# Kernel optimization log

Measured on AMD Instinct MI355X. Metric: run time of the kernel, lower is better.

Reference implementation:

```python
import jax, jax.numpy as jnp
import numpy as np

B, S = 2, 2048
H = 16
NOPE, ROPE, VD = 128, 64, 128
Q_RANK, KV_RANK = 1536, 512
SCALE = 1.0 / np.sqrt(NOPE + ROPE)  # 1/sqrt(192)
NEG_INF = -10000.0


def _make_rope(n_pos, dim):
    # matches gen_rope: theta over even indices, angles repeated twice (rotate-half layout)
    theta = 1.0 / (10000.0 ** (np.arange(0, dim, 2, dtype=np.float32) / dim))
    pos = np.arange(n_pos, dtype=np.float32)
    ang = np.outer(pos, theta)                      # [N, dim/2]
    ang = np.concatenate([ang, ang], axis=-1)       # [N, dim]
    return jnp.asarray(np.cos(ang)), jnp.asarray(np.sin(ang))


def _rope(x, cos, sin):
    # rotate-half RoPE; cos/sin broadcast over head dim if present
    d = x.shape[-1]
    x1, x2 = x[..., : d // 2], x[..., d // 2 :]
    rot = jnp.concatenate([-x2, x1], axis=-1)
    return x * cos + rot * sin


def setup_inputs() -> dict:
    key = jax.random.key(0)
    ks = jax.random.split(key, 5)
    Q = jax.random.normal(ks[0], (B, S, Q_RANK), dtype=jnp.float32)
    KV = jax.random.normal(ks[1], (B, S, KV_RANK), dtype=jnp.float32)
    PE = jax.random.normal(ks[2], (B, S, ROPE), dtype=jnp.float32)
    WUQ = jax.random.normal(ks[3], (H * (NOPE + ROPE), Q_RANK), dtype=jnp.float32) * 0.02
    WUKV = jax.random.normal(ks[4], (H * (NOPE + VD), KV_RANK), dtype=jnp.float32) * 0.02
    cos, sin = _make_rope(B * S, ROPE)
    cos = cos.reshape(B, S, ROPE)
    sin = sin.reshape(B, S, ROPE)
    mask = jnp.triu(jnp.full((S, S), NEG_INF, dtype=jnp.float32), k=1)
    return {"Q": Q, "KV": KV, "PE": PE, "WUQ": WUQ, "WUKV": WUKV,
            "cos": cos, "sin": sin, "mask": mask}


def reference(Q, KV, PE, WUQ, WUKV, cos, sin, mask):
    b, s, _ = Q.shape
    # low-rank up-projections
    q = jnp.einsum("bsl,dl->bsd", Q, WUQ).reshape(b, s, H, NOPE + ROPE)
    q_nope, q_pe = q[..., :NOPE], q[..., NOPE:]
    q_pe = _rope(q_pe, cos[:, :, None, :], sin[:, :, None, :])

    kv = jnp.einsum("bsl,dl->bsd", KV, WUKV).reshape(b, s, H, NOPE + VD)
    k_nope, v = kv[..., :NOPE], kv[..., NOPE:]
    k_pe = _rope(PE, cos, sin)  # [b, s, ROPE], shared across heads

    # attention scores: per-head nope part + shared rope part
    scores = jnp.einsum("bqhd,bkhd->bhqk", q_nope, k_nope)
    scores = scores + jnp.einsum("bqhd,bkd->bhqk", q_pe, k_pe)
    scores = scores * SCALE + mask[None, None, :, :]
    attn = jax.nn.softmax(scores, axis=-1)
    out = jnp.einsum("bhqk,bkhd->bqhd", attn, v)  # [b, s, H, VD]
    return out
```

## Files before the change

kernel.cpp:

```cpp
#include <hip/hip_runtime.h>

typedef __attribute__((ext_vector_type(8))) short short8;
typedef __attribute__((ext_vector_type(4))) float f32x4;

#define SS 2048
#define HH 16
#define NOPE_D 128
#define ROPE_D 64
#define VDIM 128
#define QD 192
#define SCALE_F 0.07216878364870323f
#define LOG2E 1.4426950408889634f

__device__ __forceinline__ unsigned short f2bf(float f) {
    unsigned int x = __builtin_bit_cast(unsigned int, f);
    unsigned int r = (x + 0x7fffu + ((x >> 16) & 1u)) >> 16;
    return (unsigned short)r;
}

#define GLDS16(g, l) __builtin_amdgcn_global_load_lds( \
    (const __attribute__((address_space(1))) void*)(g), \
    (__attribute__((address_space(3))) void*)(l), 16, 0, 0)

#define DPPF(x, ctrl) __builtin_bit_cast(float, __builtin_amdgcn_update_dpp( \
    0, __builtin_bit_cast(int, (float)(x)), (ctrl), 0xf, 0xf, true))
__device__ __forceinline__ float rowmax16(float x) {
    x = fmaxf(x, DPPF(x, 0xB1));
    x = fmaxf(x, DPPF(x, 0x4E));
    x = fmaxf(x, DPPF(x, 0x141));
    x = fmaxf(x, DPPF(x, 0x140));
    return x;
}
__device__ __forceinline__ float rowsum16(float x) {
    x += DPPF(x, 0xB1);
    x += DPPF(x, 0x4E);
    x += DPPF(x, 0x141);
    x += DPPF(x, 0x140);
    return x;
}

__global__ __launch_bounds__(256) void cvt_all(
    const float* __restrict__ Q, const float* __restrict__ WUQ,
    const float* __restrict__ KV, const float* __restrict__ WUKV,
    const float* __restrict__ PE, const float* __restrict__ cs, const float* __restrict__ sn,
    unsigned short* __restrict__ Qb, unsigned short* __restrict__ WUQb,
    unsigned short* __restrict__ KVb, unsigned short* __restrict__ WUKVb,
    unsigned short* __restrict__ kpe)
{
    int bid = blockIdx.x;
    if (bid >= 14848) {
        int idx = (bid - 14848) * 256 + threadIdx.x;
        int i = idx & 31, row = idx >> 5;
        float x1 = PE[row * 64 + i], x2 = PE[row * 64 + 32 + i];
        float c1 = cs[row * 64 + i],      s1 = sn[row * 64 + i];
        float c2 = cs[row * 64 + 32 + i], s2 = sn[row * 64 + 32 + i];
        kpe[row * 64 + i]      = f2bf(x1 * c1 - x2 * s1);
        kpe[row * 64 + 32 + i] = f2bf(x2 * c2 + x1 * s2);
        return;
    }
    const float* src; unsigned short* dst; float scale = 1.0f;
    if (bid < 6144)       { src = Q;    dst = Qb; }
    else if (bid < 10752) { src = WUQ;  dst = WUQb; bid -= 6144; scale = SCALE_F * LOG2E; }
    else if (bid < 12800) { src = KV;   dst = KVb;  bid -= 10752; }
    else                  { src = WUKV; dst = WUKVb; bid -= 12800; }
    int i = (bid * 256 + threadIdx.x) * 4;
    float4 v = *(const float4*)(src + i);
    ushort4 o = { f2bf(v.x * scale), f2bf(v.y * scale), f2bf(v.z * scale), f2bf(v.w * scale) };
    *(ushort4*)(dst + i) = o;
}

template<bool SPLIT_KV, bool ROPE>
__global__ __launch_bounds__(256) void gemm_bf16(
    const unsigned short* __restrict__ A, const unsigned short* __restrict__ B,
    unsigned short* __restrict__ C, unsigned short* __restrict__ vT,
    const float* __restrict__ cs, const float* __restrict__ sn,
    int M, int N, int K)
{
    __shared__ unsigned short As[128 * 64];
    __shared__ unsigned short Bs[128 * 64];
    const int t = threadIdx.x, w = t >> 6, lane = t & 63;
    const int n16 = lane & 15, quad = lane >> 4;
    const int bm = blockIdx.y * 128, bn = blockIdx.x * 128;
    const int wm = (w >> 1) * 64, wn = (w & 1) * 64;

    f32x4 acc[4][4] = {};

    const unsigned short* gA = A + (size_t)(bm + w * 32 + (lane >> 3)) * K + (lane & 7) * 8;
    const unsigned short* gB = B + (size_t)(bn + w * 32 + (lane >> 3)) * K + (lane & 7) * 8;

    for (int k0 = 0; k0 < K; k0 += 64) {
        __syncthreads();
        for (int j = 0; j < 4; j++) {
            GLDS16(gA + (size_t)j * 8 * K + k0, &As[(w * 32 + j * 8) * 64]);
            GLDS16(gB + (size_t)j * 8 * K + k0, &Bs[(w * 32 + j * 8) * 64]);
        }
        __syncthreads();
        for (int ks = 0; ks < 2; ks++) {
            short8 af[4], bfr[4];
            for (int mt = 0; mt < 4; mt++)
                af[mt] = *(const short8*)&As[(wm + mt * 16 + n16) * 64 + ks * 32 + quad * 8];
            for (int nt = 0; nt < 4; nt++)
                bfr[nt] = *(const short8*)&Bs[(wn + nt * 16 + n16) * 64 + ks * 32 + quad * 8];
            for (int mt = 0; mt < 4; mt++)
                for (int nt = 0; nt < 4; nt++)
                    acc[mt][nt] = __builtin_amdgcn_mfma_f32_16x16x32_bf16(af[mt], bfr[nt], acc[mt][nt], 0, 0, 0);
        }
    }

    if (!SPLIT_KV) {
        const int colbase = bn + wn;
        const bool is_pe = ROPE && ((colbase % 192) >= 128);
        if (is_pe) {
            for (int mt = 0; mt < 4; mt++)
                for (int r = 0; r < 4; r++) {
                    int row = bm + wm + mt * 16 + quad * 4 + r;
                    const float* cr = cs + row * 64;
                    const float* sr = sn + row * 64;
                    for (int nt = 0; nt < 2; nt++) {
                        int i = nt * 16 + n16;
                        float x1 = acc[mt][nt][r], x2 = acc[mt][nt + 2][r];
                        float o1 = x1 * cr[i] - x2 * sr[i];
                        float o2 = x2 * cr[32 + i] + x1 * sr[32 + i];
                        C[(size_t)row * N + colbase + i] = f2bf(o1);
                        C[(size_t)row * N + colbase + 32 + i] = f2bf(o2);
                    }
                }
        } else {
            for (int mt = 0; mt < 4; mt++)
                for (int nt = 0; nt < 4; nt++)
                    for (int r = 0; r < 4; r++)
                        C[(size_t)(bm + wm + mt * 16 + quad * 4 + r) * N + colbase + nt * 16 + n16]
                            = f2bf(acc[mt][nt][r]);
        }
    } else {
        const int colbase = bn + wn;
        if ((colbase & 255) < 128) {
            for (int mt = 0; mt < 4; mt++)
                for (int nt = 0; nt < 4; nt++) {
                    int col = colbase + nt * 16 + n16;
                    int h = col >> 8, d = col & 255;
                    for (int r = 0; r < 4; r++)
                        C[(size_t)(bm + wm + mt * 16 + quad * 4 + r) * 2048 + h * 128 + d]
                            = f2bf(acc[mt][nt][r]);
                }
        } else {
            for (int mt = 0; mt < 4; mt++)
                for (int nt = 0; nt < 4; nt++) {
                    int col = colbase + nt * 16 + n16;
                    int h = col >> 8, vd = (col & 255) - 128;
                    int row0 = bm + wm + mt * 16 + quad * 4;
                    int b = row0 >> 11, s = row0 & 2047;
                    ushort4 pk = { f2bf(acc[mt][nt][0]), f2bf(acc[mt][nt][1]),
                                   f2bf(acc[mt][nt][2]), f2bf(acc[mt][nt][3]) };
                    *(ushort4*)&vT[((size_t)(b * 16 + h) * 128 + vd) * 2048 + s] = pk;
                }
        }
    }
}

__global__ __launch_bounds__(256, 2) void attn_kernel(
    const unsigned short* __restrict__ qbuf,
    const unsigned short* __restrict__ knope,
    const unsigned short* __restrict__ kpe,
    const unsigned short* __restrict__ vT,
    float* __restrict__ out)
{
    const int bid = blockIdx.x;
    int qt, c;
    if (bid < 256) { qt = 15 - (bid >> 5); c = bid & 31; }
    else           { qt = (bid - 256) >> 5; c = bid & 31; }
    const int h = c & 15, b = c >> 4;
    const int t = threadIdx.x, w = t >> 6, lane = t & 63;
    const int n16 = lane & 15, quad = lane >> 4;

    __shared__ unsigned short Kn[64 * 128];
    __shared__ unsigned short Kp[64 * 64];
    __shared__ unsigned short Vt[128 * 64];
    __shared__ unsigned short Ps[4][32 * 72];

    const unsigned short* knb = knope + (size_t)b * 2048 * 2048 + h * 128;
    const unsigned short* kpb = kpe + (size_t)b * 2048 * 64;
    const unsigned short* vtb = vT + (size_t)(b * 16 + h) * 128 * 2048;

    short8 qf[2][6];
    for (int mt = 0; mt < 2; mt++) {
        size_t grow = (size_t)(b * SS + qt * 128 + w * 32 + mt * 16 + n16);
        const unsigned short* qp = qbuf + grow * (HH * QD) + h * QD + quad * 8;
        for (int ks = 0; ks < 6; ks++) qf[mt][ks] = *(const short8*)(qp + ks * 32);
    }

    f32x4 O[2][8] = {};
    float m_i[2][4], ps[2][4];
    for (int mt = 0; mt < 2; mt++)
        for (int r = 0; r < 4; r++) { m_i[mt][r] = -INFINITY; ps[mt][r] = 0.f; }

    const int nkt = 2 * qt + 2;
    for (int kt = 0; kt < nkt; kt++) {
        __syncthreads();
        {
            int r = w * 16 + (lane >> 4);
            int sl = lane & 15;
            for (int j = 0; j < 4; j++) {
                int rr = r + j * 4;
                const unsigned short* g = knb + (size_t)(kt * 64 + rr) * 2048 + ((sl ^ (rr & 7)) * 8);
                GLDS16(g, &Kn[(w * 16 + j * 4) * 128]);
            }
        }
        {
            int r = w * 16 + (lane >> 3);
            int sl = lane & 7;
            for (int j = 0; j < 2; j++) {
                int rr = r + j * 8;
                const unsigned short* g = kpb + (size_t)(kt * 64 + rr) * 64 + ((sl ^ (rr & 7)) * 8);
                GLDS16(g, &Kp[(w * 16 + j * 8) * 64]);
            }
        }
        {
            int r = w * 32 + (lane >> 3);
            int sl = lane & 7;
            for (int j = 0; j < 4; j++) {
                int rr = r + j * 8;
                const unsigned short* g = vtb + (size_t)rr * 2048 + kt * 64 + ((sl ^ (rr & 7)) * 8);
                GLDS16(g, &Vt[(w * 32 + j * 8) * 64]);
            }
        }
        __syncthreads();

        f32x4 Sg[2][4];
        for (int nt = 0; nt < 4; nt++) {
            int key = nt * 16 + n16, kx = key & 7;
            f32x4 a0 = {}, a1 = {};
            for (int ks = 0; ks < 4; ks++) {
                short8 bfr = *(const short8*)&Kn[key * 128 + (((ks * 4 + quad) ^ kx) * 8)];
                a0 = __builtin_amdgcn_mfma_f32_16x16x32_bf16(qf[0][ks], bfr, a0, 0, 0, 0);
                a1 = __builtin_amdgcn_mfma_f32_16x16x32_bf16(qf[1][ks], bfr, a1, 0, 0, 0);
            }
            for (int ks = 0; ks < 2; ks++) {
                short8 bfr = *(const short8*)&Kp[key * 64 + (((ks * 4 + quad) ^ kx) * 8)];
                a0 = __builtin_amdgcn_mfma_f32_16x16x32_bf16(qf[0][4 + ks], bfr, a0, 0, 0, 0);
                a1 = __builtin_amdgcn_mfma_f32_16x16x32_bf16(qf[1][4 + ks], bfr, a1, 0, 0, 0);
            }
            Sg[0][nt] = a0; Sg[1][nt] = a1;
        }

        const bool edge = (kt >= 2 * qt);
        for (int mt = 0; mt < 2; mt++) {
            if (edge) {
                int rowg = qt * 128 + w * 32 + mt * 16 + quad * 4;
                for (int nt = 0; nt < 4; nt++) {
                    int colg = kt * 64 + nt * 16 + n16;
                    for (int r = 0; r < 4; r++)
                        if (colg > rowg + r) Sg[mt][nt][r] = -INFINITY;
                }
            }
            for (int r = 0; r < 4; r++) {
                float mx = fmaxf(fmaxf(Sg[mt][0][r], Sg[mt][1][r]),
                                 fmaxf(Sg[mt][2][r], Sg[mt][3][r]));
                mx = rowmax16(mx);
                float mnew = fmaxf(m_i[mt][r], mx);
                float alpha = exp2f(m_i[mt][r] - mnew);
                m_i[mt][r] = mnew;
                float rs = 0.f;
                for (int nt = 0; nt < 4; nt++) {
                    float pv = exp2f(Sg[mt][nt][r] - mnew);
                    Sg[mt][nt][r] = pv;
                    rs += pv;
                }
                ps[mt][r] = ps[mt][r] * alpha + rs;
                for (int v8 = 0; v8 < 8; v8++) O[mt][v8][r] *= alpha;
            }
            for (int nt = 0; nt < 4; nt++)
                for (int r = 0; r < 4; r++)
                    Ps[w][(mt * 16 + quad * 4 + r) * 72 + nt * 16 + n16] = f2bf(Sg[mt][nt][r]);
        }
        for (int ks = 0; ks < 2; ks++) {
            short8 pa0 = *(const short8*)&Ps[w][(0 + n16) * 72 + ks * 32 + quad * 8];
            short8 pa1 = *(const short8*)&Ps[w][(16 + n16) * 72 + ks * 32 + quad * 8];
            for (int v8 = 0; v8 < 8; v8++) {
                int vd = v8 * 16 + n16;
                short8 vb = *(const short8*)&Vt[vd * 64 + (((ks * 4 + quad) ^ (vd & 7)) * 8)];
                O[0][v8] = __builtin_amdgcn_mfma_f32_16x16x32_bf16(pa0, vb, O[0][v8], 0, 0, 0);
                O[1][v8] = __builtin_amdgcn_mfma_f32_16x16x32_bf16(pa1, vb, O[1][v8], 0, 0, 0);
            }
        }
    }

    for (int mt = 0; mt < 2; mt++)
        for (int r = 0; r < 4; r++) {
            float inv = 1.f / rowsum16(ps[mt][r]);
            size_t qrow = (size_t)(b * SS + qt * 128 + w * 32 + mt * 16 + quad * 4 + r);
            float* op = out + (qrow * HH + h) * VDIM;
            for (int v8 = 0; v8 < 8; v8++)
                op[v8 * 16 + n16] = O[mt][v8][r] * inv;
        }
}

extern "C" void kernel_launch(void* const* d_in, const int* in_sizes, int n_in,
                              void* d_out, int out_size, void* d_ws, size_t ws_size,
                              hipStream_t stream) {
    const float* Q    = (const float*)d_in[0];
    const float* KV   = (const float*)d_in[1];
    const float* PE   = (const float*)d_in[2];
    const float* WUQ  = (const float*)d_in[3];
    const float* WUKV = (const float*)d_in[4];
    const float* cosp = (const float*)d_in[5];
    const float* sinp = (const float*)d_in[6];
    float* out = (float*)d_out;

    unsigned short* qbuf  = (unsigned short*)d_ws;
    unsigned short* knope = qbuf  + (size_t)4096 * 3072;
    unsigned short* vT    = knope + (size_t)4096 * 2048;
    unsigned short* kpe   = vT    + (size_t)4096 * 2048;
    unsigned short* Qb    = kpe   + (size_t)4096 * 64;
    unsigned short* WUQb  = Qb    + (size_t)4096 * 1536;
    unsigned short* KVb   = WUQb  + (size_t)3072 * 1536;
    unsigned short* WUKVb = KVb   + (size_t)4096 * 512;

    cvt_all<<<15360, 256, 0, stream>>>(Q, WUQ, KV, WUKV, PE, cosp, sinp,
                                       Qb, WUQb, KVb, WUKVb, kpe);
    gemm_bf16<false, true><<<dim3(24, 32), 256, 0, stream>>>(
        Qb, WUQb, qbuf, nullptr, cosp, sinp, 4096, 3072, 1536);
    gemm_bf16<true, false><<<dim3(32, 32), 256, 0, stream>>>(
        KVb, WUKVb, knope, vT, nullptr, nullptr, 4096, 4096, 512);
    attn_kernel<<<512, 256, 0, stream>>>(qbuf, knope, kpe, vT, out);
}
```

Baseline: 338.8 us.

## Fuse up-projection GEMMs, swizzle LDS, and schedule attention tiles via atomic queue

The two up-projection GEMMs are merged into one launch, and their LDS tiles get an XOR swizzle to reduce bank conflicts. The attention kernel now pulls work units from a global atomic counter, longest tiles first, instead of using a fixed block mapping. It computes S transposed (K as the A operand), so the P fragments can be packed straight from registers rather than round-tripped through LDS. To match that, vT is written with a permuted sequence order, and the softmax row reductions switch from DPP to cross-quad shuffles with alpha broadcast through shared memory. The added memset and atomic loop cost a little and depend on the permuted V layout matching the packed P register order exactly.

```diff
diff --git a/kernel.cpp b/kernel.cpp
--- a/kernel.cpp
+++ b/kernel.cpp
@@ -21,23 +21,6 @@
 #define GLDS16(g, l) __builtin_amdgcn_global_load_lds( \
     (const __attribute__((address_space(1))) void*)(g), \
     (__attribute__((address_space(3))) void*)(l), 16, 0, 0)
-
-#define DPPF(x, ctrl) __builtin_bit_cast(float, __builtin_amdgcn_update_dpp( \
-    0, __builtin_bit_cast(int, (float)(x)), (ctrl), 0xf, 0xf, true))
-__device__ __forceinline__ float rowmax16(float x) {
-    x = fmaxf(x, DPPF(x, 0xB1));
-    x = fmaxf(x, DPPF(x, 0x4E));
-    x = fmaxf(x, DPPF(x, 0x141));
-    x = fmaxf(x, DPPF(x, 0x140));
-    return x;
-}
-__device__ __forceinline__ float rowsum16(float x) {
-    x += DPPF(x, 0xB1);
-    x += DPPF(x, 0x4E);
-    x += DPPF(x, 0x141);
-    x += DPPF(x, 0x140);
-    return x;
-}
 
 __global__ __launch_bounds__(256) void cvt_all(
     const float* __restrict__ Q, const float* __restrict__ WUQ,
@@ -69,24 +52,32 @@
     *(ushort4*)(dst + i) = o;
 }
 
-template<bool SPLIT_KV, bool ROPE>
-__global__ __launch_bounds__(256) void gemm_bf16(
-    const unsigned short* __restrict__ A, const unsigned short* __restrict__ B,
-    unsigned short* __restrict__ C, unsigned short* __restrict__ vT,
-    const float* __restrict__ cs, const float* __restrict__ sn,
-    int M, int N, int K)
+__global__ __launch_bounds__(256) void gemm_fused(
+    const unsigned short* __restrict__ Qb, const unsigned short* __restrict__ WUQb,
+    const unsigned short* __restrict__ KVb, const unsigned short* __restrict__ WUKVb,
+    unsigned short* __restrict__ qbuf, unsigned short* __restrict__ knope,
+    unsigned short* __restrict__ vT,
+    const float* __restrict__ cs, const float* __restrict__ sn)
 {
     __shared__ unsigned short As[128 * 64];
     __shared__ unsigned short Bs[128 * 64];
     const int t = threadIdx.x, w = t >> 6, lane = t & 63;
     const int n16 = lane & 15, quad = lane >> 4;
-    const int bm = blockIdx.y * 128, bn = blockIdx.x * 128;
+
+    int bid = blockIdx.x;
+    const unsigned short *A, *B; int N, K, bm, bn; bool g1;
+    if (bid < 768) { g1 = true;  A = Qb;  B = WUQb;  N = 3072; K = 1536;
+                     bm = (bid / 24) * 128; bn = (bid % 24) * 128; }
+    else           { g1 = false; bid -= 768; A = KVb; B = WUKVb; N = 4096; K = 512;
+                     bm = (bid / 32) * 128; bn = (bid % 32) * 128; }
+
     const int wm = (w >> 1) * 64, wn = (w & 1) * 64;
-
     f32x4 acc[4][4] = {};
 
-    const unsigned short* gA = A + (size_t)(bm + w * 32 + (lane >> 3)) * K + (lane & 7) * 8;
-    const unsigned short* gB = B + (size_t)(bn + w * 32 + (lane >> 3)) * K + (lane & 7) * 8;
+    const int lr = lane >> 3, lc = lane & 7;
+    const int sw = (lc ^ lr) * 8;
+    const unsigned short* gA = A + (size_t)(bm + w * 32 + lr) * K + sw;
+    const unsigned short* gB = B + (size_t)(bn + w * 32 + lr) * K + sw;
 
     for (int k0 = 0; k0 < K; k0 += 64) {
         __syncthreads();
@@ -96,20 +87,24 @@
         }
         __syncthreads();
         for (int ks = 0; ks < 2; ks++) {
-            short8 af[4], bfr[4];
-            for (int mt = 0; mt < 4; mt++)
-                af[mt] = *(const short8*)&As[(wm + mt * 16 + n16) * 64 + ks * 32 + quad * 8];
-            for (int nt = 0; nt < 4; nt++)
-                bfr[nt] = *(const short8*)&Bs[(wn + nt * 16 + n16) * 64 + ks * 32 + quad * 8];
+            short8 af[4], bf[4];
+            for (int mt = 0; mt < 4; mt++) {
+                int rw = wm + mt * 16 + n16;
+                af[mt] = *(const short8*)&As[rw * 64 + (((ks * 4 + quad) ^ (rw & 7)) * 8)];
+            }
+            for (int nt = 0; nt < 4; nt++) {
+                int rw = wn + nt * 16 + n16;
+                bf[nt] = *(const short8*)&Bs[rw * 64 + (((ks * 4 + quad) ^ (rw & 7)) * 8)];
+            }
             for (int mt = 0; mt < 4; mt++)
                 for (int nt = 0; nt < 4; nt++)
-                    acc[mt][nt] = __builtin_amdgcn_mfma_f32_16x16x32_bf16(af[mt], bfr[nt], acc[mt][nt], 0, 0, 0);
+                    acc[mt][nt] = __builtin_amdgcn_mfma_f32_16x16x32_bf16(af[mt], bf[nt], acc[mt][nt], 0, 0, 0);
         }
     }
 
-    if (!SPLIT_KV) {
-        const int colbase = bn + wn;
-        const bool is_pe = ROPE && ((colbase % 192) >= 128);
+    const int colbase = bn + wn;
+    if (g1) {
+        const bool is_pe = ((colbase % 192) >= 128);
         if (is_pe) {
             for (int mt = 0; mt < 4; mt++)
                 for (int r = 0; r < 4; r++) {
@@ -121,26 +116,25 @@
                         float x1 = acc[mt][nt][r], x2 = acc[mt][nt + 2][r];
                         float o1 = x1 * cr[i] - x2 * sr[i];
                         float o2 = x2 * cr[32 + i] + x1 * sr[32 + i];
-                        C[(size_t)row * N + colbase + i] = f2bf(o1);
-                        C[(size_t)row * N + colbase + 32 + i] = f2bf(o2);
+                        qbuf[(size_t)row * N + colbase + i] = f2bf(o1);
+                        qbuf[(size_t)row * N + colbase + 32 + i] = f2bf(o2);
                     }
                 }
         } else {
             for (int mt = 0; mt < 4; mt++)
                 for (int nt = 0; nt < 4; nt++)
                     for (int r = 0; r < 4; r++)
-                        C[(size_t)(bm + wm + mt * 16 + quad * 4 + r) * N + colbase + nt * 16 + n16]
+                        qbuf[(size_t)(bm + wm + mt * 16 + quad * 4 + r) * N + colbase + nt * 16 + n16]
                             = f2bf(acc[mt][nt][r]);
         }
     } else {
-        const int colbase = bn + wn;
         if ((colbase & 255) < 128) {
             for (int mt = 0; mt < 4; mt++)
                 for (int nt = 0; nt < 4; nt++) {
                     int col = colbase + nt * 16 + n16;
                     int h = col >> 8, d = col & 255;
                     for (int r = 0; r < 4; r++)
-                        C[(size_t)(bm + wm + mt * 16 + quad * 4 + r) * 2048 + h * 128 + d]
+                        knope[(size_t)(bm + wm + mt * 16 + quad * 4 + r) * 2048 + h * 128 + d]
                             = f2bf(acc[mt][nt][r]);
                 }
         } else {
@@ -149,10 +143,13 @@
                     int col = colbase + nt * 16 + n16;
                     int h = col >> 8, vd = (col & 255) - 128;
                     int row0 = bm + wm + mt * 16 + quad * 4;
-                    int b = row0 >> 11, s = row0 & 2047;
+                    int b = row0 >> 11, s0 = row0 & 2047;
+                    int l6 = s0 & 63;
+                    int scol = (s0 & ~63) + ((l6 >> 5) & 1) * 32 + ((l6 >> 2) & 3) * 8
+                             + ((l6 >> 4) & 1) * 4 + (l6 & 3);
                     ushort4 pk = { f2bf(acc[mt][nt][0]), f2bf(acc[mt][nt][1]),
                                    f2bf(acc[mt][nt][2]), f2bf(acc[mt][nt][3]) };
-                    *(ushort4*)&vT[((size_t)(b * 16 + h) * 128 + vd) * 2048 + s] = pk;
+                    *(ushort4*)&vT[((size_t)(b * 16 + h) * 128 + vd) * 2048 + scol] = pk;
                 }
         }
     }
@@ -163,136 +160,167 @@
     const unsigned short* __restrict__ knope,
     const unsigned short* __restrict__ kpe,
     const unsigned short* __restrict__ vT,
-    float* __restrict__ out)
+    float* __restrict__ out,
+    int* __restrict__ qc)
 {
-    const int bid = blockIdx.x;
-    int qt, c;
-    if (bid < 256) { qt = 15 - (bid >> 5); c = bid & 31; }
-    else           { qt = (bid - 256) >> 5; c = bid & 31; }
-    const int h = c & 15, b = c >> 4;
     const int t = threadIdx.x, w = t >> 6, lane = t & 63;
     const int n16 = lane & 15, quad = lane >> 4;
 
     __shared__ unsigned short Kn[64 * 128];
     __shared__ unsigned short Kp[64 * 64];
     __shared__ unsigned short Vt[128 * 64];
-    __shared__ unsigned short Ps[4][32 * 72];
-
-    const unsigned short* knb = knope + (size_t)b * 2048 * 2048 + h * 128;
-    const unsigned short* kpb = kpe + (size_t)b * 2048 * 64;
-    const unsigned short* vtb = vT + (size_t)(b * 16 + h) * 128 * 2048;
-
-    short8 qf[2][6];
-    for (int mt = 0; mt < 2; mt++) {
-        size_t grow = (size_t)(b * SS + qt * 128 + w * 32 + mt * 16 + n16);
-        const unsigned short* qp = qbuf + grow * (HH * QD) + h * QD + quad * 8;
-        for (int ks = 0; ks < 6; ks++) qf[mt][ks] = *(const short8*)(qp + ks * 32);
+    __shared__ float Al[4][32];
+    __shared__ int su;
+
+    while (true) {
+        __syncthreads();
+        if (t == 0) su = atomicAdd(qc, 1);
+        __syncthreads();
+        const int u = su;
+        if (u >= 512) break;
+        const int qt = 15 - (u >> 5);
+        const int c = u & 31;
+        const int h = c & 15, b = c >> 4;
+
+        const unsigned short* knb = knope + (size_t)b * 2048 * 2048 + h * 128;
+        const unsigned short* kpb = kpe + (size_t)b * 2048 * 64;
+        const unsigned short* vtb = vT + (size_t)(b * 16 + h) * 128 * 2048;
+
+        short8 qf[2][6];
+        for (int qg = 0; qg < 2; qg++) {
+            size_t grow = (size_t)(b * SS + qt * 128 + w * 32 + qg * 16 + n16);
+            const unsigned short* qp = qbuf + grow * (HH * QD) + h * QD + quad * 8;
+            for (int ks = 0; ks < 6; ks++) qf[qg][ks] = *(const short8*)(qp + ks * 32);
+        }
+
+        f32x4 O[2][8] = {};
+        float m_i[2] = { -INFINITY, -INFINITY };
+        float l_i[2] = { 0.f, 0.f };
+
+        const int nkt = 2 * qt + 2;
+        for (int kt = 0; kt < nkt; kt++) {
+            __syncthreads();
+            {
+                int r = w * 16 + (lane >> 4);
+                int sl = lane & 15;
+                for (int j = 0; j < 4; j++) {
+                    int rr = r + j * 4;
+                    const unsigned short* g = knb + (size_t)(kt * 64 + rr) * 2048 + ((sl ^ (rr & 7)) * 8);
+                    GLDS16(g, &Kn[(w * 16 + j * 4) * 128]);
+                }
+            }
+            {
+                int r = w * 16 + (lane >> 3);
+                int sl = lane & 7;
+                for (int j = 0; j < 2; j++) {
+                    int rr = r + j * 8;
+                    const unsigned short* g = kpb + (size_t)(kt * 64 + rr) * 64 + ((sl ^ (rr & 7)) * 8);
+                    GLDS16(g, &Kp[(w * 16 + j * 8) * 64]);
+                }
+            }
+            {
+                int r = w * 32 + (lane >> 3);
+                int sl = lane & 7;
+                for (int j = 0; j < 4; j++) {
+                    int rr = r + j * 8;
+                    const unsigned short* g = vtb + (size_t)rr * 2048 + kt * 64 + ((sl ^ (rr & 7)) * 8);
+                    GLDS16(g, &Vt[(w * 32 + j * 8) * 64]);
+                }
+            }
+            __syncthreads();
+
+            f32x4 Sg[2][4];
+            for (int nt = 0; nt < 4; nt++) {
+                int key = nt * 16 + n16, kx = key & 7;
+                f32x4 a0 = {}, a1 = {};
+                for (int ks = 0; ks < 4; ks++) {
+                    short8 af = *(const short8*)&Kn[key * 128 + (((ks * 4 + quad) ^ kx) * 8)];
+                    a0 = __builtin_amdgcn_mfma_f32_16x16x32_bf16(af, qf[0][ks], a0, 0, 0, 0);
+                    a1 = __builtin_amdgcn_mfma_f32_16x16x32_bf16(af, qf[1][ks], a1, 0, 0, 0);
+                }
+                for (int ks = 0; ks < 2; ks++) {
+                    short8 af = *(const short8*)&Kp[key * 64 + (((ks * 4 + quad) ^ kx) * 8)];
+                    a0 = __builtin_amdgcn_mfma_f32_16x16x32_bf16(af, qf[0][4 + ks], a0, 0, 0, 0);
+                    a1 = __builtin_amdgcn_mfma_f32_16x16x32_bf16(af, qf[1][4 + ks], a1, 0, 0, 0);
+                }
+                Sg[0][nt] = a0; Sg[1][nt] = a1;
+            }
+
+            if (kt >= 2 * qt) {
+                for (int qg = 0; qg < 2; qg++) {
+                    int qq = qt * 128 + w * 32 + qg * 16 + n16;
+                    for (int nt = 0; nt < 4; nt++) {
+                        int key0 = kt * 64 + nt * 16 + quad * 4;
+                        for (int r = 0; r < 4; r++)
+                            if (key0 + r > qq) Sg[qg][nt][r] = -INFINITY;
+                    }
+                }
+            }
+
+            float alpha[2];
+            for (int qg = 0; qg < 2; qg++) {
+                float mx = -INFINITY;
+                for (int nt = 0; nt < 4; nt++)
+                    for (int r = 0; r < 4; r++) mx = fmaxf(mx, Sg[qg][nt][r]);
+                mx = fmaxf(mx, __shfl_xor(mx, 16, 64));
+                mx = fmaxf(mx, __shfl_xor(mx, 32, 64));
+                float mnew = fmaxf(m_i[qg], mx);
+                alpha[qg] = exp2f(m_i[qg] - mnew);
+                m_i[qg] = mnew;
+                float rs = 0.f;
+                for (int nt = 0; nt < 4; nt++)
+                    for (int r = 0; r < 4; r++) {
+                        float pv = exp2f(Sg[qg][nt][r] - mnew);
+                        Sg[qg][nt][r] = pv;
+                        rs += pv;
+                    }
+                l_i[qg] = l_i[qg] * alpha[qg] + rs;
+            }
+            if (quad == 0) { Al[w][n16] = alpha[0]; Al[w][16 + n16] = alpha[1]; }
+            f32x4 av0 = *(const f32x4*)&Al[w][quad * 4];
+            f32x4 av1 = *(const f32x4*)&Al[w][16 + quad * 4];
+            for (int v8 = 0; v8 < 8; v8++)
+                for (int r = 0; r < 4; r++) {
+                    O[0][v8][r] *= av0[r];
+                    O[1][v8][r] *= av1[r];
+                }
+
+            short8 pp[2][2];
+            for (int qg = 0; qg < 2; qg++)
+                for (int ntp = 0; ntp < 2; ntp++) {
+                    short8 pa;
+                    for (int j = 0; j < 4; j++) pa[j] = (short)f2bf(Sg[qg][ntp * 2][j]);
+                    for (int j = 0; j < 4; j++) pa[4 + j] = (short)f2bf(Sg[qg][ntp * 2 + 1][j]);
+                    pp[qg][ntp] = pa;
+                }
+            for (int ntp = 0; ntp < 2; ntp++)
+                for (int v8 = 0; v8 < 8; v8++) {
+                    int vd = v8 * 16 + n16;
+                    short8 vb = *(const short8*)&Vt[vd * 64 + (((ntp * 4 + quad) ^ (vd & 7)) * 8)];
+                    O[0][v8] = __builtin_amdgcn_mfma_f32_16x16x32_bf16(pp[0][ntp], vb, O[0][v8], 0, 0, 0);
+                    O[1][v8] = __builtin_amdgcn_mfma_f32_16x16x32_bf16(pp[1][ntp], vb, O[1][v8], 0, 0, 0);
+                }
+        }
+
+        {
+            float l0 = l_i[0];
+            l0 += __shfl_xor(l0, 16, 64); l0 += __shfl_xor(l0, 32, 64);
+            float l1 = l_i[1];
+            l1 += __shfl_xor(l1, 16, 64); l1 += __shfl_xor(l1, 32, 64);
+            if (quad == 0) { Al[w][n16] = 1.f / l0; Al[w][16 + n16] = 1.f / l1; }
+        }
+        f32x4 lv0 = *(const f32x4*)&Al[w][quad * 4];
+        f32x4 lv1 = *(const f32x4*)&Al[w][16 + quad * 4];
+        for (int qg = 0; qg < 2; qg++) {
+            const f32x4 lv = qg ? lv1 : lv0;
+            for (int r = 0; r < 4; r++) {
+                size_t qrow = (size_t)(b * SS + qt * 128 + w * 32 + qg * 16 + quad * 4 + r);
+                float* op = out + (qrow * HH + h) * VDIM;
+                for (int v8 = 0; v8 < 8; v8++)
+                    op[v8 * 16 + n16] = O[qg][v8][r] * lv[r];
+            }
+        }
     }
-
-    f32x4 O[2][8] = {};
-    float m_i[2][4], ps[2][4];
-    for (int mt = 0; mt < 2; mt++)
-        for (int r = 0; r < 4; r++) { m_i[mt][r] = -INFINITY; ps[mt][r] = 0.f; }
-
-    const int nkt = 2 * qt + 2;
-    for (int kt = 0; kt < nkt; kt++) {
-        __syncthreads();
-        {
-            int r = w * 16 + (lane >> 4);
-            int sl = lane & 15;
-            for (int j = 0; j < 4; j++) {
-                int rr = r + j * 4;
-                const unsigned short* g = knb + (size_t)(kt * 64 + rr) * 2048 + ((sl ^ (rr & 7)) * 8);
-                GLDS16(g, &Kn[(w * 16 + j * 4) * 128]);
-            }
-        }
-        {
-            int r = w * 16 + (lane >> 3);
-            int sl = lane & 7;
-            for (int j = 0; j < 2; j++) {
-                int rr = r + j * 8;
-                const unsigned short* g = kpb + (size_t)(kt * 64 + rr) * 64 + ((sl ^ (rr & 7)) * 8);
-                GLDS16(g, &Kp[(w * 16 + j * 8) * 64]);
-            }
-        }
-        {
-            int r = w * 32 + (lane >> 3);
-            int sl = lane & 7;
-            for (int j = 0; j < 4; j++) {
-                int rr = r + j * 8;
-                const unsigned short* g = vtb + (size_t)rr * 2048 + kt * 64 + ((sl ^ (rr & 7)) * 8);
-                GLDS16(g, &Vt[(w * 32 + j * 8) * 64]);
-            }
-        }
-        __syncthreads();
-
-        f32x4 Sg[2][4];
-        for (int nt = 0; nt < 4; nt++) {
-            int key = nt * 16 + n16, kx = key & 7;
-            f32x4 a0 = {}, a1 = {};
-            for (int ks = 0; ks < 4; ks++) {
-                short8 bfr = *(const short8*)&Kn[key * 128 + (((ks * 4 + quad) ^ kx) * 8)];
-                a0 = __builtin_amdgcn_mfma_f32_16x16x32_bf16(qf[0][ks], bfr, a0, 0, 0, 0);
-                a1 = __builtin_amdgcn_mfma_f32_16x16x32_bf16(qf[1][ks], bfr, a1, 0, 0, 0);
-            }
-            for (int ks = 0; ks < 2; ks++) {
-                short8 bfr = *(const short8*)&Kp[key * 64 + (((ks * 4 + quad) ^ kx) * 8)];
-                a0 = __builtin_amdgcn_mfma_f32_16x16x32_bf16(qf[0][4 + ks], bfr, a0, 0, 0, 0);
-                a1 = __builtin_amdgcn_mfma_f32_16x16x32_bf16(qf[1][4 + ks], bfr, a1, 0, 0, 0);
-            }
-            Sg[0][nt] = a0; Sg[1][nt] = a1;
-        }
-
-        const bool edge = (kt >= 2 * qt);
-        for (int mt = 0; mt < 2; mt++) {
-            if (edge) {
-                int rowg = qt * 128 + w * 32 + mt * 16 + quad * 4;
-                for (int nt = 0; nt < 4; nt++) {
-                    int colg = kt * 64 + nt * 16 + n16;
-                    for (int r = 0; r < 4; r++)
-                        if (colg > rowg + r) Sg[mt][nt][r] = -INFINITY;
-                }
-            }
-            for (int r = 0; r < 4; r++) {
-                float mx = fmaxf(fmaxf(Sg[mt][0][r], Sg[mt][1][r]),
-                                 fmaxf(Sg[mt][2][r], Sg[mt][3][r]));
-                mx = rowmax16(mx);
-                float mnew = fmaxf(m_i[mt][r], mx);
-                float alpha = exp2f(m_i[mt][r] - mnew);
-                m_i[mt][r] = mnew;
-                float rs = 0.f;
-                for (int nt = 0; nt < 4; nt++) {
-                    float pv = exp2f(Sg[mt][nt][r] - mnew);
-                    Sg[mt][nt][r] = pv;
-                    rs += pv;
-                }
-                ps[mt][r] = ps[mt][r] * alpha + rs;
-                for (int v8 = 0; v8 < 8; v8++) O[mt][v8][r] *= alpha;
-            }
-            for (int nt = 0; nt < 4; nt++)
-                for (int r = 0; r < 4; r++)
-                    Ps[w][(mt * 16 + quad * 4 + r) * 72 + nt * 16 + n16] = f2bf(Sg[mt][nt][r]);
-        }
-        for (int ks = 0; ks < 2; ks++) {
-            short8 pa0 = *(const short8*)&Ps[w][(0 + n16) * 72 + ks * 32 + quad * 8];
-            short8 pa1 = *(const short8*)&Ps[w][(16 + n16) * 72 + ks * 32 + quad * 8];
-            for (int v8 = 0; v8 < 8; v8++) {
-                int vd = v8 * 16 + n16;
-                short8 vb = *(const short8*)&Vt[vd * 64 + (((ks * 4 + quad) ^ (vd & 7)) * 8)];
-                O[0][v8] = __builtin_amdgcn_mfma_f32_16x16x32_bf16(pa0, vb, O[0][v8], 0, 0, 0);
-                O[1][v8] = __builtin_amdgcn_mfma_f32_16x16x32_bf16(pa1, vb, O[1][v8], 0, 0, 0);
-            }
-        }
-    }
-
-    for (int mt = 0; mt < 2; mt++)
-        for (int r = 0; r < 4; r++) {
-            float inv = 1.f / rowsum16(ps[mt][r]);
-            size_t qrow = (size_t)(b * SS + qt * 128 + w * 32 + mt * 16 + quad * 4 + r);
-            float* op = out + (qrow * HH + h) * VDIM;
-            for (int v8 = 0; v8 < 8; v8++)
-                op[v8 * 16 + n16] = O[mt][v8][r] * inv;
-        }
 }
 
 extern "C" void kernel_launch(void* const* d_in, const int* in_sizes, int n_in,
@@ -315,12 +343,12 @@
     unsigned short* WUQb  = Qb    + (size_t)4096 * 1536;
     unsigned short* KVb   = WUQb  + (size_t)3072 * 1536;
     unsigned short* WUKVb = KVb   + (size_t)4096 * 512;
-
+    int* qcounter = (int*)(WUKVb + (size_t)4096 * 512);
+
+    hipMemsetAsync(qcounter, 0, 4, stream);
     cvt_all<<<15360, 256, 0, stream>>>(Q, WUQ, KV, WUKV, PE, cosp, sinp,
                                        Qb, WUQb, KVb, WUKVb, kpe);
-    gemm_bf16<false, true><<<dim3(24, 32), 256, 0, stream>>>(
-        Qb, WUQb, qbuf, nullptr, cosp, sinp, 4096, 3072, 1536);
-    gemm_bf16<true, false><<<dim3(32, 32), 256, 0, stream>>>(
-        KVb, WUKVb, knope, vT, nullptr, nullptr, 4096, 4096, 512);
-    attn_kernel<<<512, 256, 0, stream>>>(qbuf, knope, kpe, vT, out);
-}
+    gemm_fused<<<1792, 256, 0, stream>>>(Qb, WUQb, KVb, WUKVb,
+                                         qbuf, knope, vT, cosp, sinp);
+    attn_kernel<<<512, 256, 0, stream>>>(qbuf, knope, kpe, vT, out, qcounter);
+}
```

Measured after the change: 302.3 us. -10.8%, faster.
